# Kernel tuning notes

Hardware: AMD Instinct MI355X
Metric: run time of the kernel (lower is better)

The kernel has to match this reference:

```python
import jax, jax.numpy as jnp
import numpy as np

N = 400000
D = 512
NS = 50000


def setup_inputs() -> dict:
    key = jax.random.key(0)
    k1, k2, k3, k4 = jax.random.split(key, 4)
    x = jax.random.normal(k1, (N, D), dtype=jnp.float32)
    index = jax.random.randint(k2, (N,), 0, NS, dtype=jnp.int64)
    Wg = jax.random.normal(k3, (D, 1), dtype=jnp.float32) / np.sqrt(D)
    bg = jnp.zeros((1,), dtype=jnp.float32)
    Wm = jax.random.normal(k4, (D, D), dtype=jnp.float32) / np.sqrt(D)
    bm = jnp.zeros((D,), dtype=jnp.float32)
    return {"x": x, "index": index, "Wg": Wg, "bg": bg, "Wm": Wm, "bm": bm,
            "num_segments": NS}


def reference(x, index, Wg, bg, Wm, bm, num_segments):
    # gate_nn: Linear(D, 1)
    gate = x @ Wg + bg                                   # [N, 1]
    # segment softmax over nodes sharing an index (stable via segment max)
    gmax = jax.ops.segment_max(gate, index, num_segments=num_segments)  # [NS, 1]
    gate = jnp.exp(gate - gmax[index])                   # [N, 1]
    gsum = jax.ops.segment_sum(gate, index, num_segments=num_segments)  # [NS, 1]
    gate = gate / (gsum[index] + 1e-10)                  # [N, 1]
    # message_nn: Linear(D, D)
    m = x @ Wm + bm                                      # [N, D]
    out = jax.ops.segment_sum(gate * m, index, num_segments=num_segments)  # [NS, D]
    return out
```

## Files before the change

### kernel.cpp

```cpp
#include <hip/hip_runtime.h>
#include <hip/hip_bf16.h>

#define NROWS 400000
#define DDIM  512
#define NSEG  50000

typedef __bf16 bf16x8 __attribute__((ext_vector_type(8)));
typedef float  f32x4_t __attribute__((ext_vector_type(4)));

#define GLOAD_LDS16(gsrc, ldst)                                                  \
    __builtin_amdgcn_global_load_lds(                                            \
        (const __attribute__((address_space(1))) void*)(gsrc),                   \
        (__attribute__((address_space(3))) void*)(ldst), 16, 0, 0)


__global__ __launch_bounds__(256)
void count_and_prep(const int* __restrict__ idx, int* __restrict__ counts,
                    const float* __restrict__ Wm, __bf16* __restrict__ WmT) {
    __shared__ float tile[64 * 65];
    int b = blockIdx.x;
    int t = threadIdx.x;
    if (b < 1563) {
        int r = b * 256 + t;
        if (r < NROWS) atomicAdd(&counts[idx[r]], 1);
    } else {
        int tb = b - 1563;
        int kt = tb >> 3, nt = tb & 7;
        int cc = t & 63, rg = t >> 6;
#pragma unroll
        for (int it = 0; it < 16; ++it) {
            int rr = it * 4 + rg;
            tile[rr * 65 + cc] = Wm[(size_t)(kt * 64 + rr) * 512 + nt * 64 + cc];
        }
        __syncthreads();
#pragma unroll
        for (int it = 0; it < 16; ++it) {
            int nn = it * 4 + rg;
            WmT[(size_t)(nt * 64 + nn) * 512 + kt * 64 + cc] =
                (__bf16)tile[cc * 65 + nn];
        }
    }
}


__global__ __launch_bounds__(1024)
void scan_kernel(const int* __restrict__ counts, int* __restrict__ offsets,
                 int* __restrict__ cursor) {
    __shared__ int waveSums[16];
    const int t = threadIdx.x;
    const int lane = t & 63;
    const int w = t >> 6;
    const int base = w * 3125;
    const int end  = base + 3125;

    int s = 0;
    for (int j = base + lane; j < end; j += 64) s += counts[j];
#pragma unroll
    for (int d = 1; d < 64; d <<= 1) s += __shfl_xor(s, d);
    if (lane == 0) waveSums[w] = s;
    __syncthreads();
    if (t == 0) {
        int run = 0;
#pragma unroll
        for (int i = 0; i < 16; ++i) { int v = waveSums[i]; waveSums[i] = run; run += v; }
    }
    __syncthreads();
    int run = waveSums[w];

    for (int j0 = base; j0 < end; j0 += 64) {
        int j = j0 + lane;
        int c = (j < end) ? counts[j] : 0;
        int inc = c;
#pragma unroll
        for (int d = 1; d < 64; d <<= 1) {
            int v = __shfl_up(inc, d);
            if (lane >= d) inc += v;
        }
        int exc = run + inc - c;
        if (j < end) { offsets[j] = exc; cursor[j] = exc; }
        run += __shfl(inc, 63);
    }
    if (t == 1023) offsets[NSEG] = NROWS;
}

__global__ void scatter_kernel(const int* __restrict__ idx, int* __restrict__ cursor,
                               int* __restrict__ sortedIds) {
    int r = blockIdx.x * 256 + threadIdx.x;
    if (r < NROWS) {
        int p = atomicAdd(&cursor[idx[r]], 1);
        sortedIds[p] = r;
    }
}


__global__ __launch_bounds__(256)
void pool_kernel(const float* __restrict__ x,
                 const int* __restrict__ offsets,
                 const int* __restrict__ sortedIds,
                 const float* __restrict__ Wg,
                 const float* __restrict__ bgp,
                 __bf16* __restrict__ px,
                 float* __restrict__ scaleB) {
    const int lane = threadIdx.x & 63;
    const int s = blockIdx.x * 4 + (threadIdx.x >> 6);
    const f32x4_t wg0 = *(const f32x4_t*)(Wg + lane * 8);
    const f32x4_t wg1 = *(const f32x4_t*)(Wg + lane * 8 + 4);
    const float bg = bgp[0];
    const int beg = offsets[s];
    const int n   = offsets[s + 1] - beg;
    const int* sid = sortedIds + beg;

    f32x4_t acc0 = {0.f, 0.f, 0.f, 0.f}, acc1 = acc0;
    float gs = 0.f;

    f32x4_t r0a = acc0, r0b = acc0, r1a = acc0, r1b = acc0;
    f32x4_t r2a = acc0, r2b = acc0, r3a = acc0, r3b = acc0;

#define LOADR(k, u0, u1)                                                        \
    {   const float* xr = x + (size_t)sid[k] * DDIM + lane * 8;                 \
        u0 = __builtin_nontemporal_load((const f32x4_t*)xr);                    \
        u1 = __builtin_nontemporal_load((const f32x4_t*)(xr + 4)); }
#define COMPR(u0, u1)                                                           \
    {   float p = u0.x * wg0.x + u0.y * wg0.y + u0.z * wg0.z + u0.w * wg0.w     \
                + u1.x * wg1.x + u1.y * wg1.y + u1.z * wg1.z + u1.w * wg1.w;    \
        p += __shfl_xor(p, 1);  p += __shfl_xor(p, 2);  p += __shfl_xor(p, 4);  \
        p += __shfl_xor(p, 8);  p += __shfl_xor(p, 16); p += __shfl_xor(p, 32); \
        float e = __expf(p + bg);                                               \
        gs += e; acc0 += e * u0; acc1 += e * u1; }

    if (n > 0) LOADR(0, r0a, r0b);
    if (n > 1) LOADR(1, r1a, r1b);
    if (n > 2) LOADR(2, r2a, r2b);
    if (n > 3) LOADR(3, r3a, r3b);

    int k = 0;
    for (; k + 8 <= n; k += 4) {
        COMPR(r0a, r0b); LOADR(k + 4, r0a, r0b);
        COMPR(r1a, r1b); LOADR(k + 5, r1a, r1b);
        COMPR(r2a, r2b); LOADR(k + 6, r2a, r2b);
        COMPR(r3a, r3b); LOADR(k + 7, r3a, r3b);
    }
    {
        int rem = n - k;
        if (rem > 0) COMPR(r0a, r0b);
        if (rem > 4) LOADR(k + 4, r0a, r0b);
        if (rem > 1) COMPR(r1a, r1b);
        if (rem > 5) LOADR(k + 5, r1a, r1b);
        if (rem > 2) COMPR(r2a, r2b);
        if (rem > 6) LOADR(k + 6, r2a, r2b);
        if (rem > 3) COMPR(r3a, r3b);
        if (rem > 4) COMPR(r0a, r0b);
        if (rem > 5) COMPR(r1a, r1b);
        if (rem > 6) COMPR(r2a, r2b);
    }
#undef LOADR
#undef COMPR

    float inv = 1.f / (gs + 1e-10f);
    bf16x8 o;
    o[0] = (__bf16)(acc0.x * inv); o[1] = (__bf16)(acc0.y * inv);
    o[2] = (__bf16)(acc0.z * inv); o[3] = (__bf16)(acc0.w * inv);
    o[4] = (__bf16)(acc1.x * inv); o[5] = (__bf16)(acc1.y * inv);
    o[6] = (__bf16)(acc1.z * inv); o[7] = (__bf16)(acc1.w * inv);
    *(bf16x8*)(px + (size_t)s * DDIM + lane * 8) = o;
    if (lane == 0) scaleB[s] = gs * inv;
}


__global__ __launch_bounds__(256)
void gemm_out(const __bf16* __restrict__ px,
              const __bf16* __restrict__ WmT,
              const float* __restrict__ bm,
              const float* __restrict__ scaleB,
              float* __restrict__ out) {
    __shared__ __align__(16) __bf16 As[128 * 64];
    __shared__ __align__(16) __bf16 Bs[128 * 64];

    const int t     = threadIdx.x;
    const int lane  = t & 63;
    const int w     = t >> 6;
    const int ntile = blockIdx.x & 3;
    const int mtile = blockIdx.x >> 2;

    const int kq = lane & 15;
    const int rq = lane >> 4;
    const int wr = w >> 1;
    const int wc = w & 1;

    const char* srcA[4];
    const char* srcB[4];
    int ldsOff[4];
#pragma unroll
    for (int q = 0; q < 4; ++q) {
        int base = w * 4096 + q * 1024;
        int L = base + lane * 16;
        int r = L >> 7;
        int c = (L & 127) ^ ((r & 7) << 4);
        ldsOff[q] = base;
        int growA = mtile * 128 + r; if (growA >= NSEG) growA = NSEG - 1;
        srcA[q] = (const char*)px + (size_t)growA * 1024 + c;
        srcB[q] = (const char*)WmT + (size_t)(ntile * 128 + r) * 1024 + c;
    }

    f32x4_t acc[4][4];
#pragma unroll
    for (int i = 0; i < 4; ++i)
#pragma unroll
        for (int j = 0; j < 4; ++j)
            acc[i][j] = f32x4_t{0.f, 0.f, 0.f, 0.f};

    for (int ks = 0; ks < 8; ++ks) {
#pragma unroll
        for (int q = 0; q < 4; ++q) {
            GLOAD_LDS16(srcA[q] + ks * 128, (char*)As + ldsOff[q]);
            GLOAD_LDS16(srcB[q] + ks * 128, (char*)Bs + ldsOff[q]);
        }
        asm volatile("s_waitcnt vmcnt(0)" ::: "memory");
        __builtin_amdgcn_s_barrier();
#pragma unroll
        for (int kk = 0; kk < 2; ++kk) {
            int kbyte = rq * 16 + kk * 64;
            bf16x8 a[4], b[4];
#pragma unroll
            for (int mi = 0; mi < 4; ++mi) {
                int r = wr * 64 + mi * 16 + kq;
                a[mi] = *(const bf16x8*)((char*)As + ((r * 128 + kbyte) ^ ((r & 7) << 4)));
            }
#pragma unroll
            for (int ni = 0; ni < 4; ++ni) {
                int c = wc * 64 + ni * 16 + kq;
                b[ni] = *(const bf16x8*)((char*)Bs + ((c * 128 + kbyte) ^ ((c & 7) << 4)));
            }
#pragma unroll
            for (int mi = 0; mi < 4; ++mi)
#pragma unroll
                for (int ni = 0; ni < 4; ++ni)
                    acc[mi][ni] = __builtin_amdgcn_mfma_f32_16x16x32_bf16(
                        a[mi], b[ni], acc[mi][ni], 0, 0, 0);
        }
        __builtin_amdgcn_s_barrier();
    }

#pragma unroll
    for (int mi = 0; mi < 4; ++mi) {
#pragma unroll
        for (int j = 0; j < 4; ++j) {
            int rrow = wr * 64 + mi * 16 + rq * 4 + j;
            int grow = mtile * 128 + rrow;
            if (grow < NSEG) {
                float sb = scaleB[grow];
                float* op = out + (size_t)grow * DDIM + ntile * 128 + wc * 64 + kq;
                const float* bp = bm + ntile * 128 + wc * 64 + kq;
#pragma unroll
                for (int ni = 0; ni < 4; ++ni)
                    __builtin_nontemporal_store(acc[mi][ni][j] + bp[ni * 16] * sb,
                                                op + ni * 16);
            }
        }
    }
}

extern "C" void kernel_launch(void* const* d_in, const int* in_sizes, int n_in,
                              void* d_out, int out_size, void* d_ws, size_t ws_size,
                              hipStream_t stream) {
    const float* x   = (const float*)d_in[0];
    const int*   idx = (const int*)d_in[1];
    const float* Wg  = (const float*)d_in[2];
    const float* bg  = (const float*)d_in[3];
    const float* Wm  = (const float*)d_in[4];
    const float* bm  = (const float*)d_in[5];
    float* out = (float*)d_out;

    char* W = (char*)d_ws;
    int*    counts    = (int*)   (W + 0);
    int*    offsets   = (int*)   (W + 200704);
    int*    cursor    = (int*)   (W + 401408);
    float*  scaleB    = (float*) (W + 602112);
    __bf16* WmT       = (__bf16*)(W + 802816);
    int*    sortedIds = (int*)   (W + 1327104);
    __bf16* px        = (__bf16*)(W + 2927104);

    hipMemsetAsync(counts, 0, NSEG * sizeof(int), stream);

    count_and_prep<<<1563 + 64, 256, 0, stream>>>(idx, counts, Wm, WmT);
    scan_kernel<<<1, 1024, 0, stream>>>(counts, offsets, cursor);
    scatter_kernel<<<(NROWS + 255) / 256, 256, 0, stream>>>(idx, cursor, sortedIds);

    pool_kernel<<<NSEG / 4, 256, 0, stream>>>(x, offsets, sortedIds, Wg, bg, px, scaleB);

    int mtiles = (NSEG + 127) / 128;
    gemm_out<<<mtiles * 4, 256, 0, stream>>>(px, WmT, bm, scaleB, out);
}
```

Baseline: 327.3 us.

## Fuse histogram, scan and weight transpose into one kernel with LDS histogram

Replaces the memset, global-atomic count kernel and separate scan kernel with one kernel. Block 0 builds the segment histogram in LDS using packed 16-bit counters and then scans it, while 16 other blocks transpose Wm to bf16. This removes two launches, a memset and global atomics, but serializes 400k index reads and LDS atomics through a single 1024-thread block. The 16-bit counters overflow if any segment holds more than 65535 rows.

```diff
diff --git a/kernel.cpp b/kernel.cpp
--- a/kernel.cpp
+++ b/kernel.cpp
@@ -14,73 +14,81 @@
         (__attribute__((address_space(3))) void*)(ldst), 16, 0, 0)
 
 
-__global__ __launch_bounds__(256)
-void count_and_prep(const int* __restrict__ idx, int* __restrict__ counts,
+__global__ __launch_bounds__(1024)
+void hist_scan_prep(const int* __restrict__ idx,
+                    int* __restrict__ offsets, int* __restrict__ cursor,
                     const float* __restrict__ Wm, __bf16* __restrict__ WmT) {
-    __shared__ float tile[64 * 65];
-    int b = blockIdx.x;
-    int t = threadIdx.x;
-    if (b < 1563) {
-        int r = b * 256 + t;
-        if (r < NROWS) atomicAdd(&counts[idx[r]], 1);
-    } else {
-        int tb = b - 1563;
-        int kt = tb >> 3, nt = tb & 7;
-        int cc = t & 63, rg = t >> 6;
-#pragma unroll
-        for (int it = 0; it < 16; ++it) {
-            int rr = it * 4 + rg;
-            tile[rr * 65 + cc] = Wm[(size_t)(kt * 64 + rr) * 512 + nt * 64 + cc];
-        }
-        __syncthreads();
-#pragma unroll
-        for (int it = 0; it < 16; ++it) {
-            int nn = it * 4 + rg;
-            WmT[(size_t)(nt * 64 + nn) * 512 + kt * 64 + cc] =
-                (__bf16)tile[cc * 65 + nn];
-        }
-    }
-}
-
-
-__global__ __launch_bounds__(1024)
-void scan_kernel(const int* __restrict__ counts, int* __restrict__ offsets,
-                 int* __restrict__ cursor) {
+    __shared__ uint smem[25600];
     __shared__ int waveSums[16];
     const int t = threadIdx.x;
-    const int lane = t & 63;
-    const int w = t >> 6;
-    const int base = w * 3125;
-    const int end  = base + 3125;
-
-    int s = 0;
-    for (int j = base + lane; j < end; j += 64) s += counts[j];
-#pragma unroll
-    for (int d = 1; d < 64; d <<= 1) s += __shfl_xor(s, d);
-    if (lane == 0) waveSums[w] = s;
-    __syncthreads();
-    if (t == 0) {
-        int run = 0;
-#pragma unroll
-        for (int i = 0; i < 16; ++i) { int v = waveSums[i]; waveSums[i] = run; run += v; }
-    }
-    __syncthreads();
-    int run = waveSums[w];
-
-    for (int j0 = base; j0 < end; j0 += 64) {
-        int j = j0 + lane;
-        int c = (j < end) ? counts[j] : 0;
-        int inc = c;
-#pragma unroll
-        for (int d = 1; d < 64; d <<= 1) {
-            int v = __shfl_up(inc, d);
-            if (lane >= d) inc += v;
-        }
-        int exc = run + inc - c;
-        if (j < end) { offsets[j] = exc; cursor[j] = exc; }
-        run += __shfl(inc, 63);
-    }
-    if (t == 1023) offsets[NSEG] = NROWS;
+    const int b = blockIdx.x;
+
+    if (b == 0) {
+        for (int i = t; i < 25000; i += 1024) smem[i] = 0u;
+        __syncthreads();
+        for (int i = t; i < NROWS; i += 1024) {
+            int s = idx[i];
+            atomicAdd(&smem[s >> 1], (s & 1) ? 65536u : 1u);
+        }
+        __syncthreads();
+
+        const int lane = t & 63;
+        const int w    = t >> 6;
+        const int base = w * 3125;
+        const int end  = base + 3125;
+
+        int s = 0;
+        for (int j = base + lane; j < end; j += 64)
+            s += (int)((smem[j >> 1] >> ((j & 1) * 16)) & 0xffffu);
+#pragma unroll
+        for (int d = 1; d < 64; d <<= 1) s += __shfl_xor(s, d);
+        if (lane == 0) waveSums[w] = s;
+        __syncthreads();
+        if (t == 0) {
+            int run = 0;
+#pragma unroll
+            for (int i = 0; i < 16; ++i) { int v = waveSums[i]; waveSums[i] = run; run += v; }
+        }
+        __syncthreads();
+        int run = waveSums[w];
+
+        for (int j0 = base; j0 < end; j0 += 64) {
+            int j = j0 + lane;
+            int c = (j < end) ? (int)((smem[j >> 1] >> ((j & 1) * 16)) & 0xffffu) : 0;
+            int inc = c;
+#pragma unroll
+            for (int d = 1; d < 64; d <<= 1) {
+                int v = __shfl_up(inc, d);
+                if (lane >= d) inc += v;
+            }
+            int exc = run + inc - c;
+            if (j < end) { offsets[j] = exc; cursor[j] = exc; }
+            run += __shfl(inc, 63);
+        }
+        if (t == 1023) offsets[NSEG] = NROWS;
+    } else {
+        float* tile = (float*)smem;
+        const int cc = t & 63;
+        const int rg = t >> 6;
+#pragma unroll
+        for (int q = 0; q < 4; ++q) {
+            int tb = (b - 1) * 4 + q;
+            int kt = tb >> 3, nt = tb & 7;
+#pragma unroll
+            for (int it = 0; it < 4; ++it) {
+                int rr = it * 16 + rg;
+                tile[rr * 65 + cc] = Wm[(size_t)(kt * 64 + rr) * 512 + nt * 64 + cc];
+            }
+            __syncthreads();
+#pragma unroll
+            for (int it = 0; it < 4; ++it) {
+                int nn = it * 16 + rg;
+                WmT[(size_t)(nt * 64 + nn) * 512 + kt * 64 + cc] =
+                    (__bf16)tile[cc * 65 + nn];
+            }
+            __syncthreads();
+        }
+    }
 }
 
 __global__ void scatter_kernel(const int* __restrict__ idx, int* __restrict__ cursor,
@@ -272,20 +280,15 @@
     float* out = (float*)d_out;
 
     char* W = (char*)d_ws;
-    int*    counts    = (int*)   (W + 0);
-    int*    offsets   = (int*)   (W + 200704);
-    int*    cursor    = (int*)   (W + 401408);
-    float*  scaleB    = (float*) (W + 602112);
-    __bf16* WmT       = (__bf16*)(W + 802816);
-    int*    sortedIds = (int*)   (W + 1327104);
-    __bf16* px        = (__bf16*)(W + 2927104);
-
-    hipMemsetAsync(counts, 0, NSEG * sizeof(int), stream);
-
-    count_and_prep<<<1563 + 64, 256, 0, stream>>>(idx, counts, Wm, WmT);
-    scan_kernel<<<1, 1024, 0, stream>>>(counts, offsets, cursor);
+    int*    offsets   = (int*)   (W + 0);
+    int*    cursor    = (int*)   (W + 200704);
+    float*  scaleB    = (float*) (W + 401408);
+    __bf16* WmT       = (__bf16*)(W + 602112);
+    int*    sortedIds = (int*)   (W + 1126400);
+    __bf16* px        = (__bf16*)(W + 2726400);
+
+    hist_scan_prep<<<17, 1024, 0, stream>>>(idx, offsets, cursor, Wm, WmT);
     scatter_kernel<<<(NROWS + 255) / 256, 256, 0, stream>>>(idx, cursor, sortedIds);
-
     pool_kernel<<<NSEG / 4, 256, 0, stream>>>(x, offsets, sortedIds, Wg, bg, px, scaleB);
 
     int mtiles = (NSEG + 127) / 128;
```

Result: slower. 418.6 us (+27.9%).
